# Performance work log

Hardware: AMD Instinct MI355X
Metric: run time of the kernel (lower is better)

The kernel has to match this reference:

```python
import jax, jax.numpy as jnp
import numpy as np

B, S, D, F, E = 4, 2048, 1024, 4096, 8

def setup_inputs() -> dict:
    key = jax.random.key(0)
    ks = jax.random.split(key, 5)
    x = jax.random.normal(ks[0], (B, S, D), dtype=jnp.float32)
    router_w = jax.random.normal(ks[1], (D, E), dtype=jnp.float32) * (D ** -0.5)
    router_b = jnp.zeros((E,), dtype=jnp.float32)
    w1 = jax.random.normal(ks[2], (E, F, D), dtype=jnp.float32) * (D ** -0.5)
    b1 = jnp.zeros((E, F), dtype=jnp.float32)
    w2 = jax.random.normal(ks[3], (E, D, F), dtype=jnp.float32) * (F ** -0.5)
    b2 = jnp.zeros((E, D), dtype=jnp.float32)
    return {"x": x, "router_w": router_w, "router_b": router_b,
            "w1": w1, "b1": b1, "w2": w2, "b2": b2}

def reference(x, router_w, router_b, w1, b1, w2, b2):
    # Router: mean over sequence, linear, softmax -> [B, E]
    routing_probs = jax.nn.softmax(jnp.mean(x, axis=1) @ router_w + router_b, axis=-1)
    # SMEAR merge weights: mean over batch -> [E] (dropout is identity, p=0)
    ew = jnp.mean(routing_probs, axis=0)
    # Batched weighted sum of stacked expert parameters (fuses the python loop)
    mw1 = jnp.einsum('e,efd->fd', ew, w1)   # [F, D]
    mb1 = ew @ b1                            # [F]
    mw2 = jnp.einsum('e,edf->df', ew, w2)   # [D, F]
    mb2 = ew @ b2                            # [D]
    # functional_call on merged expert (MLP with GELU)
    h = jax.nn.gelu(jnp.einsum('bsd,fd->bsf', x, mw1) + mb1)
    out = jnp.einsum('bsf,df->bsd', h, mw2) + mb2
    return out
```

## Files before the change

kernel.cpp:

```cpp
#include <hip/hip_runtime.h>
#include <hip/hip_bf16.h>
#include <stdint.h>

#define B_ 4
#define S_ 2048
#define D_ 1024
#define F_ 4096
#define E_ 8

typedef __attribute__((ext_vector_type(4))) float f32x4;
typedef __attribute__((ext_vector_type(8))) short bf16x8;

__device__ __forceinline__ unsigned short f2bf(float f) {
    union { float f; unsigned int u; } v; v.f = f;
    unsigned int r = v.u + 0x7fffu + ((v.u >> 16) & 1u);
    return (unsigned short)(r >> 16);
}

__device__ __forceinline__ float gelu_tanh(float x) {
    const float c0 = 0.7978845608028654f;
    const float c1 = 0.044715f;
    float x3 = x * x * x;
    return 0.5f * x * (1.0f + tanhf(c0 * (x + c1 * x3)));
}

__global__ void prep_x_kernel(const float* __restrict__ x,
                              unsigned short* __restrict__ xb,
                              float* __restrict__ xsum) {
    const int b = blockIdx.y;
    const int t = threadIdx.x;
    const int d0 = t * 4;
    const float* xbase = x + (size_t)b * S_ * D_;
    unsigned short* obase = xb + (size_t)b * S_ * D_;
    float s0 = 0.f, s1 = 0.f, s2 = 0.f, s3 = 0.f;
    for (int s = blockIdx.x; s < S_; s += gridDim.x) {
        f32x4 v = *(const f32x4*)(xbase + (size_t)s * D_ + d0);
        ushort4 o;
        o.x = f2bf(v.x); o.y = f2bf(v.y); o.z = f2bf(v.z); o.w = f2bf(v.w);
        *(ushort4*)(obase + (size_t)s * D_ + d0) = o;
        s0 += v.x; s1 += v.y; s2 += v.z; s3 += v.w;
    }
    atomicAdd(&xsum[b * D_ + d0 + 0], s0);
    atomicAdd(&xsum[b * D_ + d0 + 1], s1);
    atomicAdd(&xsum[b * D_ + d0 + 2], s2);
    atomicAdd(&xsum[b * D_ + d0 + 3], s3);
}

__global__ void router_kernel(const float* __restrict__ xsum,
                              const float* __restrict__ rw,
                              const float* __restrict__ rb,
                              float* __restrict__ ew) {
    __shared__ float logits[B_][E_];
    __shared__ float probs[B_][E_];
    const int t = threadIdx.x;
    const int b = t >> 6;
    const int e = (t >> 3) & 7;
    const int part = t & 7;
    float s = 0.f;
    const int dbeg = part * (D_ / 8);
    for (int d = dbeg; d < dbeg + D_ / 8; ++d)
        s += xsum[b * D_ + d] * rw[d * E_ + e];
    s += __shfl_down(s, 4);
    s += __shfl_down(s, 2);
    s += __shfl_down(s, 1);
    if (part == 0) logits[b][e] = s * (1.0f / S_) + rb[e];
    __syncthreads();
    if (t < B_) {
        float mx = -1e30f;
        for (int j = 0; j < E_; ++j) mx = fmaxf(mx, logits[t][j]);
        float sum = 0.f;
        float ex[E_];
        for (int j = 0; j < E_; ++j) { ex[j] = expf(logits[t][j] - mx); sum += ex[j]; }
        for (int j = 0; j < E_; ++j) probs[t][j] = ex[j] / sum;
    }
    __syncthreads();
    if (t < E_) {
        float m = 0.f;
        for (int j = 0; j < B_; ++j) m += probs[j][t];
        ew[t] = m * (1.0f / B_);
    }
}

__global__ void merge_w_kernel(const float* __restrict__ w, const float* __restrict__ ew,
                               unsigned short* __restrict__ dst, int n) {
    float e[E_];
#pragma unroll
    for (int i = 0; i < E_; ++i) e[i] = ew[i];
    const size_t total = (size_t)n >> 2;
    for (size_t q = (size_t)blockIdx.x * blockDim.x + threadIdx.x; q < total;
         q += (size_t)gridDim.x * blockDim.x) {
        f32x4 acc = {0.f, 0.f, 0.f, 0.f};
#pragma unroll
        for (int i = 0; i < E_; ++i) {
            f32x4 v = *(const f32x4*)(w + (size_t)i * n + q * 4);
            acc += v * e[i];
        }
        ushort4 o;
        o.x = f2bf(acc.x); o.y = f2bf(acc.y); o.z = f2bf(acc.z); o.w = f2bf(acc.w);
        *(ushort4*)(dst + q * 4) = o;
    }
}

__global__ void merge_b_kernel(const float* __restrict__ w, const float* __restrict__ ew,
                               float* __restrict__ dst, int n) {
    float e[E_];
#pragma unroll
    for (int i = 0; i < E_; ++i) e[i] = ew[i];
    for (int i = blockIdx.x * blockDim.x + threadIdx.x; i < n; i += gridDim.x * blockDim.x) {
        float a = 0.f;
#pragma unroll
        for (int j = 0; j < E_; ++j) a += e[j] * w[(size_t)j * n + i];
        dst[i] = a;
    }
}

template <int EPI>
__global__ __launch_bounds__(256) void gemm_nt(const unsigned short* __restrict__ A,
                                               const unsigned short* __restrict__ Bm,
                                               const float* __restrict__ bias,
                                               void* __restrict__ Cout,
                                               int M, int N, int K) {
    __shared__ unsigned short As[128 * 32];
    __shared__ unsigned short Bs[128 * 32];
    const int tid = threadIdx.x;
    const int wave = tid >> 6;
    const int lane = tid & 63;
    const int wr = wave >> 1, wc = wave & 1;
    const int row0 = blockIdx.y * 128;
    const int col0 = blockIdx.x * 128;

    const unsigned short* Ag = A + (size_t)row0 * K;
    const unsigned short* Bg = Bm + (size_t)col0 * K;

    f32x4 acc[4][4];
#pragma unroll
    for (int m = 0; m < 4; ++m)
#pragma unroll
        for (int n = 0; n < 4; ++n) acc[m][n] = (f32x4){0.f, 0.f, 0.f, 0.f};

    const int srow = wave * 32 + (lane >> 2);
    const int skoff = (lane & 3) * 8;

    for (int kt = 0; kt < K; kt += 32) {
#pragma unroll
        for (int i = 0; i < 2; ++i) {
            const unsigned short* ga = Ag + (size_t)(srow + i * 16) * K + kt + skoff;
            const unsigned short* gb = Bg + (size_t)(srow + i * 16) * K + kt + skoff;
            unsigned short* la = &As[(wave * 32 + i * 16) * 32];
            unsigned short* lb = &Bs[(wave * 32 + i * 16) * 32];
            __builtin_amdgcn_global_load_lds((const __attribute__((address_space(1))) void*)ga,
                                             (__attribute__((address_space(3))) void*)la, 16, 0, 0);
            __builtin_amdgcn_global_load_lds((const __attribute__((address_space(1))) void*)gb,
                                             (__attribute__((address_space(3))) void*)lb, 16, 0, 0);
        }
        __syncthreads();
        bf16x8 af[4], bq[4];
#pragma unroll
        for (int m = 0; m < 4; ++m)
            af[m] = *(const bf16x8*)&As[(wr * 64 + m * 16 + (lane & 15)) * 32 + (lane >> 4) * 8];
#pragma unroll
        for (int n = 0; n < 4; ++n)
            bq[n] = *(const bf16x8*)&Bs[(wc * 64 + n * 16 + (lane & 15)) * 32 + (lane >> 4) * 8];
#pragma unroll
        for (int m = 0; m < 4; ++m)
#pragma unroll
            for (int n = 0; n < 4; ++n)
                acc[m][n] = __builtin_amdgcn_mfma_f32_16x16x32_bf16(af[m], bq[n], acc[m][n], 0, 0, 0);
        __syncthreads();
    }

    const int fr = lane & 15;
    const int fq = lane >> 4;
#pragma unroll
    for (int m = 0; m < 4; ++m) {
#pragma unroll
        for (int n = 0; n < 4; ++n) {
            const int c = col0 + wc * 64 + n * 16 + fr;
            const float bv = bias[c];
#pragma unroll
            for (int v = 0; v < 4; ++v) {
                const int r = row0 + wr * 64 + m * 16 + fq * 4 + v;
                float val = acc[m][n][v] + bv;
                if (EPI == 0) {
                    ((unsigned short*)Cout)[(size_t)r * N + c] = f2bf(gelu_tanh(val));
                } else {
                    ((float*)Cout)[(size_t)r * N + c] = val;
                }
            }
        }
    }
}

extern "C" void kernel_launch(void* const* d_in, const int* in_sizes, int n_in,
                              void* d_out, int out_size, void* d_ws, size_t ws_size,
                              hipStream_t stream) {
    const float* x  = (const float*)d_in[0];
    const float* rw = (const float*)d_in[1];
    const float* rb = (const float*)d_in[2];
    const float* w1 = (const float*)d_in[3];
    const float* b1 = (const float*)d_in[4];
    const float* w2 = (const float*)d_in[5];
    const float* b2 = (const float*)d_in[6];
    float* out = (float*)d_out;

    char* p = (char*)d_ws;
    auto take = [&](size_t bytes) { char* r = p; p += (bytes + 255) & ~(size_t)255; return r; };
    float* xsum          = (float*)take((size_t)B_ * D_ * sizeof(float));
    float* ew            = (float*)take(E_ * sizeof(float));
    float* mb1           = (float*)take(F_ * sizeof(float));
    float* mb2           = (float*)take(D_ * sizeof(float));
    unsigned short* xb   = (unsigned short*)take((size_t)B_ * S_ * D_ * 2);
    unsigned short* mw1b = (unsigned short*)take((size_t)F_ * D_ * 2);
    unsigned short* mw2b = (unsigned short*)take((size_t)D_ * F_ * 2);
    unsigned short* h    = (unsigned short*)take((size_t)B_ * S_ * F_ * 2);

    hipMemsetAsync(xsum, 0, (size_t)B_ * D_ * sizeof(float), stream);
    prep_x_kernel<<<dim3(32, B_), 256, 0, stream>>>(x, xb, xsum);
    router_kernel<<<1, 256, 0, stream>>>(xsum, rw, rb, ew);
    merge_w_kernel<<<2048, 256, 0, stream>>>(w1, ew, mw1b, F_ * D_);
    merge_w_kernel<<<2048, 256, 0, stream>>>(w2, ew, mw2b, D_ * F_);
    merge_b_kernel<<<16, 256, 0, stream>>>(b1, ew, mb1, F_);
    merge_b_kernel<<<4, 256, 0, stream>>>(b2, ew, mb2, D_);
    gemm_nt<0><<<dim3(F_ / 128, (B_ * S_) / 128), 256, 0, stream>>>(xb, mw1b, mb1, h, B_ * S_, F_, D_);
    gemm_nt<1><<<dim3(D_ / 128, (B_ * S_) / 128), 256, 0, stream>>>(h, mw2b, mb2, out, B_ * S_, D_, F_);
}
```

Baseline: 615.0 us.

## Replace GEMMs with 256x256 double-buffered swizzled kernel and split-K atomics

Replaces the 128x128 single-stage GEMM with a 256x256-tile, 512-thread kernel. It uses a double-buffered LDS pipeline over 64-wide K steps, XOR-swizzled LDS layout, interleaved MFMA and load scheduling, and setprio hints. The second GEMM is split along K into two slices that atomically accumulate into an output pre-filled with the merged bias. The change also fuses the two bias-merge launches and widens the prep_x grid. The aim is higher data reuse and overlap of global loads with MFMA, at the cost of float atomics, which make the output order nondeterministic, and heavy LDS and register use.

```diff
diff --git a/kernel.cpp b/kernel.cpp
--- a/kernel.cpp
+++ b/kernel.cpp
@@ -101,94 +101,187 @@
     }
 }
 
-__global__ void merge_b_kernel(const float* __restrict__ w, const float* __restrict__ ew,
-                               float* __restrict__ dst, int n) {
+__global__ void merge_biases(const float* __restrict__ b1, const float* __restrict__ b2,
+                             const float* __restrict__ ew,
+                             float* __restrict__ mb1, float* __restrict__ mb2) {
+    const int i = blockIdx.x * blockDim.x + threadIdx.x;
     float e[E_];
 #pragma unroll
-    for (int i = 0; i < E_; ++i) e[i] = ew[i];
-    for (int i = blockIdx.x * blockDim.x + threadIdx.x; i < n; i += gridDim.x * blockDim.x) {
+    for (int j = 0; j < E_; ++j) e[j] = ew[j];
+    if (i < F_) {
         float a = 0.f;
 #pragma unroll
-        for (int j = 0; j < E_; ++j) a += e[j] * w[(size_t)j * n + i];
-        dst[i] = a;
-    }
-}
+        for (int j = 0; j < E_; ++j) a += e[j] * b1[(size_t)j * F_ + i];
+        mb1[i] = a;
+    } else if (i - F_ < D_) {
+        const int i2 = i - F_;
+        float a = 0.f;
+#pragma unroll
+        for (int j = 0; j < E_; ++j) a += e[j] * b2[(size_t)j * D_ + i2];
+        mb2[i2] = a;
+    }
+}
+
+__global__ void init_out_kernel(float* __restrict__ out, const float* __restrict__ mb2) {
+    const size_t total_q = (size_t)B_ * S_ * D_ / 4;
+    for (size_t q = (size_t)blockIdx.x * blockDim.x + threadIdx.x; q < total_q;
+         q += (size_t)gridDim.x * blockDim.x) {
+        ((f32x4*)out)[q] = ((const f32x4*)mb2)[q & (D_ / 4 - 1)];
+    }
+}
+
+#define LGKM0() do { asm volatile("s_waitcnt lgkmcnt(0)" ::: "memory"); \
+                     __builtin_amdgcn_sched_barrier(0); } while (0)
+#define VMCNT(n) asm volatile("s_waitcnt vmcnt(" #n ")" ::: "memory")
+#define BARRIER() __builtin_amdgcn_s_barrier()
 
 template <int EPI>
-__global__ __launch_bounds__(256) void gemm_nt(const unsigned short* __restrict__ A,
-                                               const unsigned short* __restrict__ Bm,
-                                               const float* __restrict__ bias,
-                                               void* __restrict__ Cout,
-                                               int M, int N, int K) {
-    __shared__ unsigned short As[128 * 32];
-    __shared__ unsigned short Bs[128 * 32];
+__global__ __launch_bounds__(512, 2) void gemm256(const unsigned short* __restrict__ A,
+                                                  const unsigned short* __restrict__ Bm,
+                                                  const float* __restrict__ bias,
+                                                  void* __restrict__ Cout0,
+                                                  int M, int N, int K, int Klen) {
+    __shared__ __align__(128) char lds[131072];
     const int tid = threadIdx.x;
-    const int wave = tid >> 6;
-    const int lane = tid & 63;
-    const int wr = wave >> 1, wc = wave & 1;
-    const int row0 = blockIdx.y * 128;
-    const int col0 = blockIdx.x * 128;
-
-    const unsigned short* Ag = A + (size_t)row0 * K;
-    const unsigned short* Bg = Bm + (size_t)col0 * K;
-
-    f32x4 acc[4][4];
-#pragma unroll
-    for (int m = 0; m < 4; ++m)
+    const int wave = tid >> 6, lane = tid & 63;
+    const int wr = wave >> 2, wc = wave & 3;
+    const int row0 = blockIdx.y * 256, col0 = blockIdx.x * 256;
+    const int kt0 = blockIdx.z * Klen;
+    const int NI = Klen / 128;
+
+    const int c0 = tid, c1 = tid + 512;
+    const int r0c = ((c0 >> 7) << 4) | ((c0 >> 2) & 15);
+    const int k0c = (((c0 >> 6) & 1) << 5) | ((((c0 & 3) << 3) ^ (((c0 >> 5) & 1) << 4)));
+    const int r1c = ((c1 >> 7) << 4) | ((c1 >> 2) & 15);
+    const int k1c = (((c1 >> 6) & 1) << 5) | ((((c1 & 3) << 3) ^ (((c1 >> 5) & 1) << 4)));
+    const size_t soff0 = (size_t)r0c * K + k0c;
+    const size_t soff1 = (size_t)r1c * K + k1c;
+
+    const unsigned short* pA0 = A + (size_t)row0 * K + kt0;
+    const unsigned short* pA1 = pA0 + (size_t)128 * K;
+    const unsigned short* pB0 = Bm + (size_t)col0 * K + kt0;
+    const unsigned short* pB1 = pB0 + (size_t)128 * K;
+
+    int lane_off = ((lane & 15) << 6) + ((lane >> 4) << 4);
+    lane_off ^= (lane & 8) << 2;
+    const int wrOff = wr * 16384;
+    const int wcOff = 32768 + (wc >> 1) * 16384 + (wc & 1) * 8192;
+
+    f32x4 acc[8][4];
+#pragma unroll
+    for (int m = 0; m < 8; ++m)
 #pragma unroll
         for (int n = 0; n < 4; ++n) acc[m][n] = (f32x4){0.f, 0.f, 0.f, 0.f};
-
-    const int srow = wave * 32 + (lane >> 2);
-    const int skoff = (lane & 3) * 8;
-
-    for (int kt = 0; kt < K; kt += 32) {
-#pragma unroll
-        for (int i = 0; i < 2; ++i) {
-            const unsigned short* ga = Ag + (size_t)(srow + i * 16) * K + kt + skoff;
-            const unsigned short* gb = Bg + (size_t)(srow + i * 16) * K + kt + skoff;
-            unsigned short* la = &As[(wave * 32 + i * 16) * 32];
-            unsigned short* lb = &Bs[(wave * 32 + i * 16) * 32];
-            __builtin_amdgcn_global_load_lds((const __attribute__((address_space(1))) void*)ga,
-                                             (__attribute__((address_space(3))) void*)la, 16, 0, 0);
-            __builtin_amdgcn_global_load_lds((const __attribute__((address_space(1))) void*)gb,
-                                             (__attribute__((address_space(3))) void*)lb, 16, 0, 0);
-        }
-        __syncthreads();
-        bf16x8 af[4], bq[4];
-#pragma unroll
-        for (int m = 0; m < 4; ++m)
-            af[m] = *(const bf16x8*)&As[(wr * 64 + m * 16 + (lane & 15)) * 32 + (lane >> 4) * 8];
-#pragma unroll
-        for (int n = 0; n < 4; ++n)
-            bq[n] = *(const bf16x8*)&Bs[(wc * 64 + n * 16 + (lane & 15)) * 32 + (lane >> 4) * 8];
-#pragma unroll
-        for (int m = 0; m < 4; ++m)
-#pragma unroll
-            for (int n = 0; n < 4; ++n)
-                acc[m][n] = __builtin_amdgcn_mfma_f32_16x16x32_bf16(af[m], bq[n], acc[m][n], 0, 0, 0);
-        __syncthreads();
-    }
-
-    const int fr = lane & 15;
-    const int fq = lane >> 4;
-#pragma unroll
-    for (int m = 0; m < 4; ++m) {
+    bf16x8 aF[4][2], bF[4][2];
+
+#define STAGE(ptr, ktb, ldsoff) do { \
+    __builtin_amdgcn_global_load_lds((const __attribute__((address_space(1))) void*)((ptr) + (ktb) + soff0), \
+        (__attribute__((address_space(3))) void*)(lds + (ldsoff) + wave * 1024), 16, 0, 0); \
+    __builtin_amdgcn_global_load_lds((const __attribute__((address_space(1))) void*)((ptr) + (ktb) + soff1), \
+        (__attribute__((address_space(3))) void*)(lds + (ldsoff) + wave * 1024 + 8192), 16, 0, 0); \
+  } while (0)
+
+#define RDA4(MB, BUFB) do { _Pragma("unroll") for (int m = 0; m < 4; ++m) { \
+    aF[m][0] = *(const bf16x8*)(lds + (BUFB) + wrOff + ((MB) + m) * 2048 + lane_off); \
+    aF[m][1] = *(const bf16x8*)(lds + (BUFB) + wrOff + ((MB) + m) * 2048 + 1024 + lane_off); } } while (0)
+
+#define RDB2(NB, BUFB) do { _Pragma("unroll") for (int n = 0; n < 2; ++n) { \
+    bF[(NB) + n][0] = *(const bf16x8*)(lds + (BUFB) + wcOff + ((NB) + n) * 2048 + lane_off); \
+    bF[(NB) + n][1] = *(const bf16x8*)(lds + (BUFB) + wcOff + ((NB) + n) * 2048 + 1024 + lane_off); } } while (0)
+
+#define MFMAQ(MB, NB) do { \
+    __builtin_amdgcn_s_setprio(1); \
+    _Pragma("unroll") for (int m = 0; m < 4; ++m) \
+    _Pragma("unroll") for (int n = 0; n < 2; ++n) \
+    _Pragma("unroll") for (int ks = 0; ks < 2; ++ks) \
+      acc[(MB) + m][(NB) + n] = __builtin_amdgcn_mfma_f32_16x16x32_bf16( \
+          aF[m][ks], bF[(NB) + n][ks], acc[(MB) + m][(NB) + n], 0, 0, 0); \
+    __builtin_amdgcn_s_setprio(0); \
+  } while (0)
+
+    STAGE(pA0, 0, 0);
+    STAGE(pA1, 0, 16384);
+    STAGE(pB0, 0, 32768);
+    STAGE(pB1, 0, 49152);
+    STAGE(pB0, 64, 65536 + 32768);
+    STAGE(pB1, 64, 65536 + 49152);
+
+    for (int i = 0; i < NI; ++i) {
+        const int t = 2 * i;
+        const int ktN1 = (t + 1) * 64, ktN2 = (t + 2) * 64, ktN3 = (t + 3) * 64;
+        const bool last = (i == NI - 1);
+
+        VMCNT(4);
+        BARRIER();
+        RDA4(0, 0); RDB2(0, 0);
+        STAGE(pA0, ktN1, 65536);
+        LGKM0();
+        MFMAQ(0, 0);
+        RDB2(2, 0);
+        STAGE(pA1, ktN1, 65536 + 16384);
+        LGKM0();
+        MFMAQ(0, 2);
+        BARRIER();
+        RDA4(4, 0);
+        if (!last) STAGE(pB0, ktN2, 32768);
+        LGKM0();
+        MFMAQ(4, 2);
+        if (!last) STAGE(pB1, ktN2, 49152);
+        MFMAQ(4, 0);
+        if (last) { VMCNT(0); } else { VMCNT(4); }
+        BARRIER();
+        RDA4(0, 65536); RDB2(0, 65536);
+        if (!last) STAGE(pA0, ktN2, 0);
+        LGKM0();
+        MFMAQ(0, 0);
+        RDB2(2, 65536);
+        if (!last) STAGE(pA1, ktN2, 16384);
+        LGKM0();
+        MFMAQ(0, 2);
+        BARRIER();
+        RDA4(4, 65536);
+        if (!last) STAGE(pB0, ktN3, 65536 + 32768);
+        LGKM0();
+        MFMAQ(4, 2);
+        if (!last) STAGE(pB1, ktN3, 65536 + 49152);
+        MFMAQ(4, 0);
+    }
+
+    const int fr = lane & 15, fq = lane >> 4;
+    if (EPI == 0) {
+        unsigned short* dst = (unsigned short*)Cout0;
 #pragma unroll
         for (int n = 0; n < 4; ++n) {
             const int c = col0 + wc * 64 + n * 16 + fr;
             const float bv = bias[c];
 #pragma unroll
-            for (int v = 0; v < 4; ++v) {
-                const int r = row0 + wr * 64 + m * 16 + fq * 4 + v;
-                float val = acc[m][n][v] + bv;
-                if (EPI == 0) {
-                    ((unsigned short*)Cout)[(size_t)r * N + c] = f2bf(gelu_tanh(val));
-                } else {
-                    ((float*)Cout)[(size_t)r * N + c] = val;
+            for (int m = 0; m < 8; ++m) {
+                const int rb = row0 + wr * 128 + m * 16 + fq * 4;
+#pragma unroll
+                for (int v = 0; v < 4; ++v) {
+                    float val = acc[m][n][v] + bv;
+                    dst[(size_t)(rb + v) * N + c] = f2bf(gelu_tanh(val));
                 }
             }
         }
-    }
+    } else {
+        float* dst = (float*)Cout0;
+#pragma unroll
+        for (int n = 0; n < 4; ++n) {
+            const int c = col0 + wc * 64 + n * 16 + fr;
+#pragma unroll
+            for (int m = 0; m < 8; ++m) {
+                const int rb = row0 + wr * 128 + m * 16 + fq * 4;
+#pragma unroll
+                for (int v = 0; v < 4; ++v)
+                    atomicAdd(&dst[(size_t)(rb + v) * N + c], acc[m][n][v]);
+            }
+        }
+    }
+#undef STAGE
+#undef RDA4
+#undef RDB2
+#undef MFMAQ
 }
 
 extern "C" void kernel_launch(void* const* d_in, const int* in_sizes, int n_in,
@@ -215,12 +308,14 @@
     unsigned short* h    = (unsigned short*)take((size_t)B_ * S_ * F_ * 2);
 
     hipMemsetAsync(xsum, 0, (size_t)B_ * D_ * sizeof(float), stream);
-    prep_x_kernel<<<dim3(32, B_), 256, 0, stream>>>(x, xb, xsum);
+    prep_x_kernel<<<dim3(128, B_), 256, 0, stream>>>(x, xb, xsum);
     router_kernel<<<1, 256, 0, stream>>>(xsum, rw, rb, ew);
     merge_w_kernel<<<2048, 256, 0, stream>>>(w1, ew, mw1b, F_ * D_);
     merge_w_kernel<<<2048, 256, 0, stream>>>(w2, ew, mw2b, D_ * F_);
-    merge_b_kernel<<<16, 256, 0, stream>>>(b1, ew, mb1, F_);
-    merge_b_kernel<<<4, 256, 0, stream>>>(b2, ew, mb2, D_);
-    gemm_nt<0><<<dim3(F_ / 128, (B_ * S_) / 128), 256, 0, stream>>>(xb, mw1b, mb1, h, B_ * S_, F_, D_);
-    gemm_nt<1><<<dim3(D_ / 128, (B_ * S_) / 128), 256, 0, stream>>>(h, mw2b, mb2, out, B_ * S_, D_, F_);
-}
+    merge_biases<<<(F_ + D_) / 256, 256, 0, stream>>>(b1, b2, ew, mb1, mb2);
+    init_out_kernel<<<2048, 256, 0, stream>>>(out, mb2);
+    gemm256<0><<<dim3(F_ / 256, (B_ * S_) / 256, 1), 512, 0, stream>>>(
+        xb, mw1b, mb1, h, B_ * S_, F_, D_, D_);
+    gemm256<3><<<dim3(D_ / 256, (B_ * S_) / 256, 2), 512, 0, stream>>>(
+        h, mw2b, nullptr, out, B_ * S_, D_, F_, F_ / 2);
+}
```

New measurement: 564.2 us. 8.3% less time.
